# Kernel tuning notes

Hardware: AMD Instinct MI355X
Metric: run time of the kernel (lower is better)

Reference implementation:

```python
import jax, jax.numpy as jnp
import numpy as np

N_NODES = 50000
N_EDGES = 800000
D_NODE = 128
D_EDGE = 64
N_GC = 2
H = 256
N_GRAPHS = 512


def setup_inputs() -> dict:
    key = jax.random.key(0)
    ks = jax.random.split(key, 32)
    s = 0.05
    inp = {
        'x': jax.random.normal(ks[0], (N_NODES, D_NODE), jnp.float32),
        'edge_index': jax.random.randint(ks[1], (2, N_EDGES), 0, N_NODES, jnp.int64 if jax.config.jax_enable_x64 else jnp.int32),
        'edge_attr': jax.random.normal(ks[2], (N_EDGES, D_EDGE), jnp.float32),
        'batch': jnp.sort(jax.random.randint(ks[3], (N_NODES,), 0, N_GRAPHS)),
    }
    zin = 2 * D_NODE + D_EDGE  # 320
    inp['conv_Wf'] = jax.random.normal(ks[4], (N_GC, D_NODE, zin), jnp.float32) * s
    inp['conv_bf'] = jnp.zeros((N_GC, D_NODE), jnp.float32)
    inp['conv_Ws'] = jax.random.normal(ks[5], (N_GC, D_NODE, zin), jnp.float32) * s
    inp['conv_bs'] = jnp.zeros((N_GC, D_NODE), jnp.float32)
    # mlp_1: Linear(128->256), ReLU, Linear(256->256), ReLU, proj Linear(256->128)
    inp['mlp1_W0'] = jax.random.normal(ks[6], (H, D_NODE), jnp.float32) * s
    inp['mlp1_b0'] = jnp.zeros((H,), jnp.float32)
    inp['mlp1_W1'] = jax.random.normal(ks[7], (H, H), jnp.float32) * s
    inp['mlp1_b1'] = jnp.zeros((H,), jnp.float32)
    inp['mlp1_Wp'] = jax.random.normal(ks[8], (D_NODE, H), jnp.float32) * s
    inp['mlp1_bp'] = jnp.zeros((D_NODE,), jnp.float32)
    # mlp_2: same structure
    inp['mlp2_W0'] = jax.random.normal(ks[9], (H, D_NODE), jnp.float32) * s
    inp['mlp2_b0'] = jnp.zeros((H,), jnp.float32)
    inp['mlp2_W1'] = jax.random.normal(ks[10], (H, H), jnp.float32) * s
    inp['mlp2_b1'] = jnp.zeros((H,), jnp.float32)
    inp['mlp2_Wp'] = jax.random.normal(ks[11], (D_NODE, H), jnp.float32) * s
    inp['mlp2_bp'] = jnp.zeros((D_NODE,), jnp.float32)
    inp['out_W'] = jax.random.normal(ks[12], (1, D_NODE), jnp.float32) * s
    inp['out_b'] = jnp.zeros((1,), jnp.float32)
    return inp


def _mlp(x, W0, b0, W1, b1, Wp, bp):
    h = jax.nn.relu(x @ W0.T + b0)
    h = jax.nn.relu(h @ W1.T + b1)
    return h @ Wp.T + bp


def _cgconv(x, src, dst, edge_attr, Wf, bf, Ws, bs):
    # z = [x_i (target), x_j (source), edge_attr]  -> [E, 2D+De]
    z = jnp.concatenate([x[dst], x[src], edge_attr], axis=-1)
    msg = jax.nn.sigmoid(z @ Wf.T + bf) * jax.nn.softplus(z @ Ws.T + bs)
    aggr = jax.ops.segment_sum(msg, dst, num_segments=x.shape[0])
    return x + aggr  # CGConv residual


def reference(x, edge_index, edge_attr, batch,
              conv_Wf, conv_bf, conv_Ws, conv_bs,
              mlp1_W0, mlp1_b0, mlp1_W1, mlp1_b1, mlp1_Wp, mlp1_bp,
              mlp2_W0, mlp2_b0, mlp2_W1, mlp2_b1, mlp2_Wp, mlp2_bp,
              out_W, out_b):
    src, dst = edge_index[0], edge_index[1]
    out = x
    for l in range(N_GC):
        out = _cgconv(out, src, dst, edge_attr, conv_Wf[l], conv_bf[l], conv_Ws[l], conv_bs[l])
    out = out + _mlp(out, mlp1_W0, mlp1_b0, mlp1_W1, mlp1_b1, mlp1_Wp, mlp1_bp)
    out = jax.ops.segment_sum(out, batch, num_segments=N_GRAPHS)  # global_add_pool
    out = out + _mlp(out, mlp2_W0, mlp2_b0, mlp2_W1, mlp2_b1, mlp2_Wp, mlp2_bp)
    out = out @ out_W.T + out_b  # [n_graphs, 1]
    return out
```

## Files before the change

kernel.cpp:

```cpp
#include <hip/hip_runtime.h>
#include <stdint.h>

#define NN 50000
#define NE 800000
#define DN 128
#define DE 64
#define NG 512
#define HD 256
#define LDA 72
#define SPK_S 130

typedef unsigned short ushort_t;
typedef __attribute__((ext_vector_type(8))) short short8;
typedef __attribute__((ext_vector_type(4))) float floatx4;

__device__ __forceinline__ float bflo(unsigned u){ unsigned v=u<<16; float f; __builtin_memcpy(&f,&v,4); return f; }
__device__ __forceinline__ float bfhi(unsigned u){ unsigned v=u&0xffff0000u; float f; __builtin_memcpy(&f,&v,4); return f; }
__device__ __forceinline__ ushort_t f2bf(float f){ unsigned u; __builtin_memcpy(&u,&f,4); u += 0x7FFFu + ((u>>16)&1u); return (ushort_t)(u>>16); }
__device__ __forceinline__ unsigned cvtpk(float a, float b){
#if __has_builtin(__builtin_amdgcn_cvt_pk_bf16_f32)
  auto r = __builtin_amdgcn_cvt_pk_bf16_f32(a,b);
  unsigned u; __builtin_memcpy(&u,&r,4); return u;
#else
  return (unsigned)f2bf(a) | ((unsigned)f2bf(b)<<16);
#endif
}

__device__ __forceinline__ float actv(float fv, float sv){
  const float L2E = 1.44269504f, LN2 = 0.69314718f;
  float ef  = __builtin_amdgcn_exp2f(-L2E*fv);
  float sig = __builtin_amdgcn_rcpf(1.f+ef);
  float t   = __builtin_amdgcn_exp2f(-L2E*fabsf(sv));
  float sp  = fmaxf(sv,0.f) + LN2*__builtin_amdgcn_logf(1.f+t);
  return sig*sp;
}

__global__ void k_prep(const float* __restrict__ Wf, const float* __restrict__ Ws,
                       const float* __restrict__ W0, const float* __restrict__ W1, const float* __restrict__ Wp,
                       const float* __restrict__ cbf, const float* __restrict__ cbs,
                       ushort_t* Wnode, ushort_t* Wedge, ushort_t* W0b, ushort_t* W1b, ushort_t* Wpb,
                       float* bias512, int* deg){
  int i = blockIdx.x*256 + threadIdx.x;
  if(i < 131072){
    int l = i >> 16, r = i & 65535;
    int n = r >> 7, k = r & 127;
    const float* W = (n<256)? Wf : Ws;
    int nn = n & 127;
    int koff = ((n>>7)&1) ? 128+k : k;
    Wnode[i] = f2bf(W[(size_t)l*128*320 + (size_t)nn*320 + koff]);
  } else if(i < 163840){
    int j = i - 131072;
    int l = j >> 14, r = j & 16383;
    int n = r >> 6, k = r & 63;
    const float* W = (n<128)? Wf : Ws;
    int nn = n & 127;
    Wedge[j] = f2bf(W[(size_t)l*128*320 + (size_t)nn*320 + 256 + k]);
  } else if(i < 196608){
    int j = i - 163840; W0b[j] = f2bf(W0[j]);
  } else if(i < 262144){
    int j = i - 196608; W1b[j] = f2bf(W1[j]);
  } else if(i < 294912){
    int j = i - 262144; Wpb[j] = f2bf(Wp[j]);
  } else if(i < 295936){
    int j = i - 294912;
    int l = j >> 9, c = j & 511;
    float v = 0.f;
    if(c < 128) v = cbf[l*128 + c];
    else if(c >= 256 && c < 384) v = cbs[l*128 + (c-256)];
    bias512[j] = v;
  } else if(i < 295936 + NN){
    deg[i - 295936] = 0;
  }
}

__global__ void k_init_x(const float* x, float* xcur, ushort_t* xb){
  int i = blockIdx.x*256 + threadIdx.x;
  if(i < NN*DN){ float v = x[i]; xcur[i]=v; xb[i]=f2bf(v); }
}

__global__ void k_zero_u32(unsigned* p, int n){
  int i = blockIdx.x*256 + threadIdx.x;
  if(i<n) p[i]=0u;
}

__global__ void k_hist(const int* dst, int* deg){
  int i = blockIdx.x*256 + threadIdx.x;
  if(i<NE) atomicAdd(&deg[dst[i]], 1);
}

__global__ void k_blocksum(const int* deg, int* bsum, int n){
  __shared__ int s[256];
  int t = threadIdx.x, i = blockIdx.x*256 + t;
  s[t] = (i<n)? deg[i] : 0;
  __syncthreads();
  for(int o=128;o>0;o>>=1){ if(t<o) s[t]+=s[t+o]; __syncthreads(); }
  if(t==0) bsum[blockIdx.x]=s[0];
}

__global__ void k_scan_bsum(int* bsum, int nb, int* offs, int nnodes){
  __shared__ int s[2][256];
  int t = threadIdx.x;
  int v = (t<nb)? bsum[t] : 0;
  s[0][t]=v; __syncthreads();
  int cur=0;
  for(int o=1;o<256;o<<=1){
    int nx=cur^1;
    s[nx][t] = s[cur][t] + ((t>=o)? s[cur][t-o] : 0);
    cur=nx; __syncthreads();
  }
  if(t<nb) bsum[t] = s[cur][t] - v;
  if(t==255) offs[nnodes] = s[cur][255];
}

__global__ void k_scanscatter(const int* deg, const int* bsum, int* offs, int* cursor, int n){
  __shared__ int s[2][256];
  int t=threadIdx.x, i=blockIdx.x*256+t;
  int v=(i<n)? deg[i] : 0;
  s[0][t]=v; __syncthreads();
  int cur=0;
  for(int o=1;o<256;o<<=1){
    int nx=cur^1;
    s[nx][t] = s[cur][t] + ((t>=o)? s[cur][t-o] : 0);
    cur=nx; __syncthreads();
  }
  if(i<n){ int ex = s[cur][t]-v + bsum[blockIdx.x]; offs[i]=ex; cursor[i]=ex; }
}

__global__ void k_scatter(const int* dst, int* cursor, int* csr_pos){
  int i = blockIdx.x*256 + threadIdx.x;
  if(i<NE){ int pos = atomicAdd(&cursor[dst[i]], 1); csr_pos[i]=pos; }
}

__global__ __launch_bounds__(256) void k_permute(const float* __restrict__ ea,
      const int* __restrict__ src_g, const int* __restrict__ dst_g,
      const int* __restrict__ csr_pos,
      ushort_t* __restrict__ eab, int* __restrict__ src_csr, int* __restrict__ dst_csr){
  int id = blockIdx.x*256 + threadIdx.x;
  if(id >= NE*8) return;
  int e = id>>3, seg = id&7;
  int pos = csr_pos[e];
  const float4* p = (const float4*)&ea[(size_t)e*64 + seg*8];
  float4 f0 = p[0], f1 = p[1];
  uint4 q;
  q.x = cvtpk(f0.x,f0.y); q.y = cvtpk(f0.z,f0.w);
  q.z = cvtpk(f1.x,f1.y); q.w = cvtpk(f1.z,f1.w);
  *(uint4*)&eab[(size_t)pos*64 + seg*8] = q;
  if(seg==0){ src_csr[pos] = src_g[e]; dst_csr[pos] = dst_g[e]; }
}

__global__ __launch_bounds__(256) void k_gemm(const ushort_t* __restrict__ Ain, const ushort_t* __restrict__ Wg,
      int M, int N, int K, const float* __restrict__ bias, int mode,
      ushort_t* __restrict__ outb, float* __restrict__ outf, const float* __restrict__ addf){
  __shared__ __align__(16) ushort_t As[64*LDA];
  __shared__ __align__(16) ushort_t Bs[64*LDA];
  int tid = threadIdx.x;
  int m0 = blockIdx.x*64, n0 = blockIdx.y*64;
  int w = tid>>6, lane = tid&63, row16 = lane&15, quad = lane>>4;
  floatx4 acc[4];
  #pragma unroll
  for(int t=0;t<4;t++) acc[t]=(floatx4)(0.f);
  int nk = K>>6;
  for(int kc=0; kc<nk; kc++){
    #pragma unroll
    for(int i=0;i<2;i++){
      int lin = tid + i*256;
      int row = lin>>3, c8 = (lin&7)*8;
      uint4 va;
      int gm = m0+row;
      if(gm < M) va = *(const uint4*)&Ain[(size_t)gm*K + kc*64 + c8];
      else va = make_uint4(0,0,0,0);
      *(uint4*)&As[row*LDA + c8] = va;
      uint4 vb = *(const uint4*)&Wg[(size_t)(n0+row)*K + kc*64 + c8];
      *(uint4*)&Bs[row*LDA + c8] = vb;
    }
    __syncthreads();
    #pragma unroll
    for(int ks=0;ks<2;ks++){
      short8 a = *(const short8*)&As[(w*16+row16)*LDA + ks*32 + quad*8];
      #pragma unroll
      for(int t=0;t<4;t++){
        short8 b = *(const short8*)&Bs[(t*16+row16)*LDA + ks*32 + quad*8];
        acc[t] = __builtin_amdgcn_mfma_f32_16x16x32_bf16(a,b,acc[t],0,0,0);
      }
    }
    __syncthreads();
  }
  #pragma unroll
  for(int t=0;t<4;t++){
    int nn = n0 + t*16 + row16;
    #pragma unroll
    for(int r=0;r<4;r++){
      int m = m0 + w*16 + quad*4 + r;
      if(m>=M) continue;
      float v = acc[t][r];
      if(bias) v += bias[nn];
      if(mode==1){ v = v>0.f? v:0.f; outb[(size_t)m*N+nn]=f2bf(v); }
      else if(mode==2){ v += addf[(size_t)m*N+nn]; outf[(size_t)m*N+nn]=v; }
      else { outb[(size_t)m*N+nn]=f2bf(v); }
    }
  }
}

__global__ __launch_bounds__(256) void k_edge_msg(const ushort_t* __restrict__ eab_g,
      const int* __restrict__ src_csr, const int* __restrict__ dst_csr,
      const ushort_t* __restrict__ Wedge, const ushort_t* __restrict__ Atab,
      ushort_t* __restrict__ msg){
  __shared__ __align__(16) char smem[40960];
  ushort_t* We  = (ushort_t*)smem;
  unsigned* spk = (unsigned*)smem;
  ushort_t* el  = (ushort_t*)(smem + 32768);

  int tid = threadIdx.x;
  int e0 = blockIdx.x*64;
  {
    const uint4* s = (const uint4*)Wedge;
    #pragma unroll
    for(int i=0;i<8;i++){
      int g = tid + i*256;
      int row = g>>3, ch = g&7;
      int pch = ch ^ (row&7);
      *(uint4*)&We[row*64 + pch*8] = s[g];
    }
  }
  {
    const uint4* s = (const uint4*)eab_g + (size_t)e0*8;
    #pragma unroll
    for(int i=0;i<2;i++){
      int g = tid + i*256;
      int row = g>>3, ch = g&7;
      int pch = ch ^ (row&7);
      *(uint4*)&el[row*64 + pch*8] = s[g];
    }
  }
  __syncthreads();

  int w = tid>>6, lane = tid&63, row16 = lane&15, quad = lane>>4;
  floatx4 acc[16];
  #pragma unroll
  for(int t=0;t<16;t++) acc[t]=(floatx4)(0.f);
  #pragma unroll
  for(int ks=0;ks<2;ks++){
    int pch = (ks*4+quad) ^ (row16&7);
    short8 a = *(const short8*)&el[(w*16+row16)*64 + pch*8];
    #pragma unroll
    for(int t=0;t<16;t++){
      short8 b = *(const short8*)&We[(t*16+row16)*64 + pch*8];
      acc[t]=__builtin_amdgcn_mfma_f32_16x16x32_bf16(a,b,acc[t],0,0,0);
    }
  }
  __syncthreads();

  #pragma unroll
  for(int t=0;t<8;t++){
    int c = t*16 + row16;
    #pragma unroll
    for(int r=0;r<4;r++){
      int rl = w*16 + quad*4 + r;
      spk[rl*SPK_S + c] = cvtpk(acc[t][r], acc[t+8][r]);
    }
  }
  __syncthreads();

  #pragma unroll
  for(int j=0;j<4;j++){
    int id  = j*256 + tid;
    int eli = id >> 4;
    int c0  = (id & 15) * 8;
    int e   = e0 + eli;
    int d = dst_csr[e], s = src_csr[e];
    const unsigned* base = &spk[eli*SPK_S + c0];
    uint4 q0 = *(const uint4*)(base);
    uint4 q1 = *(const uint4*)(base + 4);
    const ushort_t* Adp = Atab + (size_t)d*512;
    const ushort_t* Asp = Atab + (size_t)s*512;
    uint4 a0 = *(const uint4*)&Adp[c0];
    uint4 a1 = *(const uint4*)&Asp[128+c0];
    uint4 a2 = *(const uint4*)&Adp[256+c0];
    uint4 a3 = *(const uint4*)&Asp[384+c0];
    unsigned qs[8] = {q0.x,q0.y,q0.z,q0.w,q1.x,q1.y,q1.z,q1.w};
    unsigned A0[4] = {a0.x,a0.y,a0.z,a0.w};
    unsigned A1[4] = {a1.x,a1.y,a1.z,a1.w};
    unsigned A2[4] = {a2.x,a2.y,a2.z,a2.w};
    unsigned A3[4] = {a3.x,a3.y,a3.z,a3.w};
    unsigned outw[4];
    #pragma unroll
    for(int k=0;k<4;k++){
      float fv0 = bflo(qs[2*k])   + bflo(A0[k]) + bflo(A1[k]);
      float sv0 = bfhi(qs[2*k])   + bflo(A2[k]) + bflo(A3[k]);
      float fv1 = bflo(qs[2*k+1]) + bfhi(A0[k]) + bfhi(A1[k]);
      float sv1 = bfhi(qs[2*k+1]) + bfhi(A2[k]) + bfhi(A3[k]);
      outw[k] = cvtpk(actv(fv0,sv0), actv(fv1,sv1));
    }
    uint4 o4; o4.x=outw[0]; o4.y=outw[1]; o4.z=outw[2]; o4.w=outw[3];
    *(uint4*)&msg[(size_t)e*128 + c0] = o4;
  }
}

__global__ __launch_bounds__(256) void k_aggregate(const ushort_t* __restrict__ msg,
      const int* __restrict__ offs, float* __restrict__ xcur, ushort_t* __restrict__ xb){
  int v = blockIdx.x*4 + (threadIdx.x>>6);
  int lane = threadIdx.x & 63;
  int rslot = lane>>4;
  int c0 = (lane&15)*8;
  int b = offs[v], e = offs[v+1];
  float acc[8];
  #pragma unroll
  for(int k=0;k<8;k++) acc[k]=0.f;
  for(int r=b+rslot; r<e; r+=4){
    uint4 m = *(const uint4*)&msg[(size_t)r*128 + c0];
    acc[0]+=bflo(m.x); acc[1]+=bfhi(m.x);
    acc[2]+=bflo(m.y); acc[3]+=bfhi(m.y);
    acc[4]+=bflo(m.z); acc[5]+=bfhi(m.z);
    acc[6]+=bflo(m.w); acc[7]+=bfhi(m.w);
  }
  #pragma unroll
  for(int k=0;k<8;k++){
    acc[k] += __shfl_xor(acc[k],16);
    acc[k] += __shfl_xor(acc[k],32);
  }
  if(rslot==0){
    float4 x0 = *(float4*)&xcur[(size_t)v*128+c0];
    float4 x1 = *(float4*)&xcur[(size_t)v*128+c0+4];
    x0.x+=acc[0]; x0.y+=acc[1]; x0.z+=acc[2]; x0.w+=acc[3];
    x1.x+=acc[4]; x1.y+=acc[5]; x1.z+=acc[6]; x1.w+=acc[7];
    *(float4*)&xcur[(size_t)v*128+c0]=x0;
    *(float4*)&xcur[(size_t)v*128+c0+4]=x1;
    uint4 o; o.x=cvtpk(x0.x,x0.y); o.y=cvtpk(x0.z,x0.w); o.z=cvtpk(x1.x,x1.y); o.w=cvtpk(x1.z,x1.w);
    *(uint4*)&xb[(size_t)v*128+c0]=o;
  }
}

__global__ __launch_bounds__(256) void k_pool(const float* __restrict__ xcur,
      const int* __restrict__ batch, float* __restrict__ pooled){
  int b0 = blockIdx.x * 128;
  int ch = threadIdx.x & 127;
  int half = threadIdx.x >> 7;
  int n0 = b0 + half*64;
  if(n0 >= NN) return;
  int n1 = n0 + 64; if(n1 > NN) n1 = NN;
  float sum = 0.f;
  int bid = batch[n0];
  for(int n=n0; n<n1; n++){
    int b = batch[n];
    if(b != bid){ atomicAdd(&pooled[(size_t)bid*128+ch], sum); sum=0.f; bid=b; }
    sum += xcur[(size_t)n*128 + ch];
  }
  atomicAdd(&pooled[(size_t)bid*128+ch], sum);
}

__global__ __launch_bounds__(256) void k_final(const float* __restrict__ pooled,
   const float* __restrict__ W0, const float* __restrict__ b0,
   const float* __restrict__ W1, const float* __restrict__ b1,
   const float* __restrict__ Wp, const float* __restrict__ bp,
   const float* __restrict__ outW, const float* __restrict__ outB,
   float* __restrict__ out){
  __shared__ float p[128], h0[256], h1[256], red[256];
  int g = blockIdx.x, t = threadIdx.x;
  if(t<128) p[t]=pooled[(size_t)g*128+t];
  __syncthreads();
  {
    const float4* wr = (const float4*)&W0[(size_t)t*128];
    float s=0.f;
    #pragma unroll 8
    for(int k=0;k<32;k++){ float4 wv=wr[k]; s += wv.x*p[k*4]+wv.y*p[k*4+1]+wv.z*p[k*4+2]+wv.w*p[k*4+3]; }
    s += b0[t]; h0[t] = s>0.f? s:0.f;
  }
  __syncthreads();
  {
    const float4* wr = (const float4*)&W1[(size_t)t*256];
    float s=0.f;
    #pragma unroll 8
    for(int k=0;k<64;k++){ float4 wv=wr[k]; s += wv.x*h0[k*4]+wv.y*h0[k*4+1]+wv.z*h0[k*4+2]+wv.w*h0[k*4+3]; }
    s += b1[t]; h1[t] = s>0.f? s:0.f;
  }
  __syncthreads();
  float rt = 0.f;
  if(t<128){
    const float4* wr=(const float4*)&Wp[(size_t)t*256];
    float s=0.f;
    #pragma unroll 8
    for(int k=0;k<64;k++){ float4 wv=wr[k]; s += wv.x*h1[k*4]+wv.y*h1[k*4+1]+wv.z*h1[k*4+2]+wv.w*h1[k*4+3]; }
    s += bp[t] + p[t];
    rt = s * outW[t];
  }
  red[t]=rt; __syncthreads();
  for(int o=128;o>0;o>>=1){ if(t<o) red[t]+=red[t+o]; __syncthreads(); }
  if(t==0) out[g] = red[0] + outB[0];
}

extern "C" void kernel_launch(void* const* d_in, const int* in_sizes, int n_in,
                              void* d_out, int out_size, void* d_ws, size_t ws_size,
                              hipStream_t stream){
  const float* x    = (const float*)d_in[0];
  const int*   ei   = (const int*)d_in[1];
  const float* ea   = (const float*)d_in[2];
  const int*   batch= (const int*)d_in[3];
  const float* cWf  = (const float*)d_in[4];
  const float* cbf  = (const float*)d_in[5];
  const float* cWs  = (const float*)d_in[6];
  const float* cbs  = (const float*)d_in[7];
  const float* W0   = (const float*)d_in[8];
  const float* b0   = (const float*)d_in[9];
  const float* W1   = (const float*)d_in[10];
  const float* b1   = (const float*)d_in[11];
  const float* Wp   = (const float*)d_in[12];
  const float* bp   = (const float*)d_in[13];
  const float* m2W0 = (const float*)d_in[14];
  const float* m2b0 = (const float*)d_in[15];
  const float* m2W1 = (const float*)d_in[16];
  const float* m2b1 = (const float*)d_in[17];
  const float* m2Wp = (const float*)d_in[18];
  const float* m2bp = (const float*)d_in[19];
  const float* outW = (const float*)d_in[20];
  const float* outB = (const float*)d_in[21];

  const int* srcp = ei;
  const int* dstp = ei + NE;

  char* ws = (char*)d_ws;
  size_t off = 0;
  auto alloc = [&](size_t bytes)->char*{
    char* p = ws + off;
    off += (bytes + 255) & ~(size_t)255;
    return p;
  };
  float*    xcur   = (float*)   alloc((size_t)NN*DN*4);
  ushort_t* xb     = (ushort_t*)alloc((size_t)NN*DN*2);
  ushort_t* Atab   = (ushort_t*)alloc((size_t)NN*512*2);
  ushort_t* msg    = (ushort_t*)alloc((size_t)NE*128*2);
  ushort_t* eab    = (ushort_t*)alloc((size_t)NE*64*2);
  ushort_t* Wnode  = (ushort_t*)alloc((size_t)2*512*128*2);
  ushort_t* Wedge  = (ushort_t*)alloc((size_t)2*256*64*2);
  ushort_t* W0b    = (ushort_t*)alloc((size_t)256*128*2);
  ushort_t* W1b    = (ushort_t*)alloc((size_t)256*256*2);
  ushort_t* Wpb    = (ushort_t*)alloc((size_t)128*256*2);
  float*    bias512= (float*)   alloc((size_t)2*512*4);
  int*      deg    = (int*)     alloc((size_t)NN*4);
  int*      offs   = (int*)     alloc((size_t)(NN+1)*4);
  int*      cursor = (int*)     alloc((size_t)NN*4);
  int*      csr_pos= (int*)     alloc((size_t)NE*4);
  int*      src_csr= (int*)     alloc((size_t)NE*4);
  int*      dst_csr= (int*)     alloc((size_t)NE*4);
  int*      bsum   = (int*)     alloc(256*4);
  float*    pooled = (float*)   alloc((size_t)NG*DN*4);
  ushort_t* h0 = Atab;
  ushort_t* h1 = Atab + (size_t)NN*256;

  k_prep<<<(295936+NN+255)/256, 256, 0, stream>>>(cWf, cWs, W0, W1, Wp, cbf, cbs,
                                   Wnode, Wedge, W0b, W1b, Wpb, bias512, deg);
  k_init_x<<<(NN*DN+255)/256, 256, 0, stream>>>(x, xcur, xb);

  int nb = (NN+255)/256;
  k_hist<<<(NE+255)/256, 256, 0, stream>>>(dstp, deg);
  k_blocksum<<<nb, 256, 0, stream>>>(deg, bsum, NN);
  k_scan_bsum<<<1, 256, 0, stream>>>(bsum, nb, offs, NN);
  k_scanscatter<<<nb, 256, 0, stream>>>(deg, bsum, offs, cursor, NN);
  k_scatter<<<(NE+255)/256, 256, 0, stream>>>(dstp, cursor, csr_pos);
  k_permute<<<(NE*8+255)/256, 256, 0, stream>>>(ea, srcp, dstp, csr_pos, eab, src_csr, dst_csr);

  for(int l=0;l<2;l++){
    dim3 ga((NN+63)/64, 512/64);
    k_gemm<<<ga, 256, 0, stream>>>(xb, Wnode + (size_t)l*512*128, NN, 512, 128,
                                   bias512 + l*512, 0, Atab, nullptr, nullptr);
    k_edge_msg<<<NE/64, 256, 0, stream>>>(eab, src_csr, dst_csr,
                                          Wedge + (size_t)l*256*64, Atab, msg);
    k_aggregate<<<NN/4, 256, 0, stream>>>(msg, offs, xcur, xb);
  }

  {
    dim3 g0((NN+63)/64, 256/64);
    k_gemm<<<g0, 256, 0, stream>>>(xb, W0b, NN, 256, 128, b0, 1, h0, nullptr, nullptr);
    dim3 g1((NN+63)/64, 256/64);
    k_gemm<<<g1, 256, 0, stream>>>(h0, W1b, NN, 256, 256, b1, 1, h1, nullptr, nullptr);
    dim3 g2((NN+63)/64, 128/64);
    k_gemm<<<g2, 256, 0, stream>>>(h1, Wpb, NN, 128, 256, bp, 2, nullptr, xcur, xcur);
  }

  k_zero_u32<<<(NG*DN+255)/256, 256, 0, stream>>>((unsigned*)pooled, NG*DN);
  k_pool<<<(NN+127)/128, 256, 0, stream>>>(xcur, batch, pooled);

  k_final<<<NG, 256, 0, stream>>>(pooled, m2W0, m2b0, m2W1, m2b1, m2Wp, m2bp,
                                  outW, outB, (float*)d_out);
  (void)in_sizes; (void)n_in; (void)out_size; (void)ws_size;
}
```

Before: 1.090 ms.

## Fuse edge aggregation into message kernel with segmented atomics, drop msg buffer

The edge message kernel now reduces the messages of consecutive dst-sorted edges in registers and adds them straight into xcur with float atomics. This removes the separate aggregate kernel and the large bf16 msg buffer that was written and then read back each layer. The edge-attribute permutation is folded into the first layer's message kernel through an edge-id gather, and the node GEMM now reads fp32 xcur and converts to bf16 on load, so the xb copy is gone. The shared-memory stride also changes. In exchange, summation order becomes nondeterministic and atomic traffic rises when a destination's edges span several groups.

```diff
diff --git a/kernel.cpp b/kernel.cpp
--- a/kernel.cpp
+++ b/kernel.cpp
@@ -8,7 +8,7 @@
 #define NG 512
 #define HD 256
 #define LDA 72
-#define SPK_S 130
+#define SPK_S 132
 
 typedef unsigned short ushort_t;
 typedef __attribute__((ext_vector_type(8))) short short8;
@@ -33,6 +33,10 @@
   float t   = __builtin_amdgcn_exp2f(-L2E*fabsf(sv));
   float sp  = fmaxf(sv,0.f) + LN2*__builtin_amdgcn_logf(1.f+t);
   return sig*sp;
+}
+
+__device__ __forceinline__ void atomAddF(float* p, float v){
+  unsafeAtomicAdd(p, v);
 }
 
 __global__ void k_prep(const float* __restrict__ Wf, const float* __restrict__ Ws,
@@ -73,9 +77,9 @@
   }
 }
 
-__global__ void k_init_x(const float* x, float* xcur, ushort_t* xb){
+__global__ void k_init_x(const float* x, float* xcur){
   int i = blockIdx.x*256 + threadIdx.x;
-  if(i < NN*DN){ float v = x[i]; xcur[i]=v; xb[i]=f2bf(v); }
+  if(i < NN*DN) xcur[i] = x[i];
 }
 
 __global__ void k_zero_u32(unsigned* p, int n){
@@ -126,29 +130,20 @@
   if(i<n){ int ex = s[cur][t]-v + bsum[blockIdx.x]; offs[i]=ex; cursor[i]=ex; }
 }
 
-__global__ void k_scatter(const int* dst, int* cursor, int* csr_pos){
+__global__ void k_scatter(const int* dst, const int* src, int* cursor,
+                          int* eid, int* src_csr, int* dst_csr){
   int i = blockIdx.x*256 + threadIdx.x;
-  if(i<NE){ int pos = atomicAdd(&cursor[dst[i]], 1); csr_pos[i]=pos; }
-}
-
-__global__ __launch_bounds__(256) void k_permute(const float* __restrict__ ea,
-      const int* __restrict__ src_g, const int* __restrict__ dst_g,
-      const int* __restrict__ csr_pos,
-      ushort_t* __restrict__ eab, int* __restrict__ src_csr, int* __restrict__ dst_csr){
-  int id = blockIdx.x*256 + threadIdx.x;
-  if(id >= NE*8) return;
-  int e = id>>3, seg = id&7;
-  int pos = csr_pos[e];
-  const float4* p = (const float4*)&ea[(size_t)e*64 + seg*8];
-  float4 f0 = p[0], f1 = p[1];
-  uint4 q;
-  q.x = cvtpk(f0.x,f0.y); q.y = cvtpk(f0.z,f0.w);
-  q.z = cvtpk(f1.x,f1.y); q.w = cvtpk(f1.z,f1.w);
-  *(uint4*)&eab[(size_t)pos*64 + seg*8] = q;
-  if(seg==0){ src_csr[pos] = src_g[e]; dst_csr[pos] = dst_g[e]; }
-}
-
-__global__ __launch_bounds__(256) void k_gemm(const ushort_t* __restrict__ Ain, const ushort_t* __restrict__ Wg,
+  if(i<NE){
+    int d = dst[i];
+    int pos = atomicAdd(&cursor[d], 1);
+    eid[pos] = i;
+    src_csr[pos] = src[i];
+    dst_csr[pos] = d;
+  }
+}
+
+__global__ __launch_bounds__(256) void k_gemm(const ushort_t* __restrict__ Ain,
+      const float* __restrict__ Af, const ushort_t* __restrict__ Wg,
       int M, int N, int K, const float* __restrict__ bias, int mode,
       ushort_t* __restrict__ outb, float* __restrict__ outf, const float* __restrict__ addf){
   __shared__ __align__(16) ushort_t As[64*LDA];
@@ -165,10 +160,18 @@
     for(int i=0;i<2;i++){
       int lin = tid + i*256;
       int row = lin>>3, c8 = (lin&7)*8;
-      uint4 va;
       int gm = m0+row;
-      if(gm < M) va = *(const uint4*)&Ain[(size_t)gm*K + kc*64 + c8];
-      else va = make_uint4(0,0,0,0);
+      uint4 va = make_uint4(0,0,0,0);
+      if(gm < M){
+        if(Af){
+          const float4* pf = (const float4*)&Af[(size_t)gm*K + kc*64 + c8];
+          float4 f0 = pf[0], f1 = pf[1];
+          va.x = cvtpk(f0.x,f0.y); va.y = cvtpk(f0.z,f0.w);
+          va.z = cvtpk(f1.x,f1.y); va.w = cvtpk(f1.z,f1.w);
+        } else {
+          va = *(const uint4*)&Ain[(size_t)gm*K + kc*64 + c8];
+        }
+      }
       *(uint4*)&As[row*LDA + c8] = va;
       uint4 vb = *(const uint4*)&Wg[(size_t)(n0+row)*K + kc*64 + c8];
       *(uint4*)&Bs[row*LDA + c8] = vb;
@@ -201,10 +204,11 @@
   }
 }
 
-__global__ __launch_bounds__(256) void k_edge_msg(const ushort_t* __restrict__ eab_g,
+__global__ __launch_bounds__(256) void k_edge_msg(const ushort_t* __restrict__ eab,
+      const float* __restrict__ ea, const int* __restrict__ eid,
       const int* __restrict__ src_csr, const int* __restrict__ dst_csr,
       const ushort_t* __restrict__ Wedge, const ushort_t* __restrict__ Atab,
-      ushort_t* __restrict__ msg){
+      float* __restrict__ xcur, ushort_t* __restrict__ eab_out, int first){
   __shared__ __align__(16) char smem[40960];
   ushort_t* We  = (ushort_t*)smem;
   unsigned* spk = (unsigned*)smem;
@@ -222,8 +226,23 @@
       *(uint4*)&We[row*64 + pch*8] = s[g];
     }
   }
-  {
-    const uint4* s = (const uint4*)eab_g + (size_t)e0*8;
+  if(first){
+    #pragma unroll
+    for(int i=0;i<2;i++){
+      int g = tid + i*256;
+      int row = g>>3, seg = g&7;
+      int eo = eid[e0+row];
+      const float4* p = (const float4*)&ea[(size_t)eo*64 + seg*8];
+      float4 f0 = p[0], f1 = p[1];
+      uint4 q;
+      q.x = cvtpk(f0.x,f0.y); q.y = cvtpk(f0.z,f0.w);
+      q.z = cvtpk(f1.x,f1.y); q.w = cvtpk(f1.z,f1.w);
+      int pch = seg ^ (row&7);
+      *(uint4*)&el[row*64 + pch*8] = q;
+      *(uint4*)&eab_out[(size_t)(e0+row)*64 + seg*8] = q;
+    }
+  } else {
+    const uint4* s = (const uint4*)eab + (size_t)e0*8;
     #pragma unroll
     for(int i=0;i<2;i++){
       int g = tid + i*256;
@@ -261,72 +280,54 @@
   }
   __syncthreads();
 
-  #pragma unroll
-  for(int j=0;j<4;j++){
-    int id  = j*256 + tid;
-    int eli = id >> 4;
-    int c0  = (id & 15) * 8;
-    int e   = e0 + eli;
-    int d = dst_csr[e], s = src_csr[e];
-    const unsigned* base = &spk[eli*SPK_S + c0];
-    uint4 q0 = *(const uint4*)(base);
-    uint4 q1 = *(const uint4*)(base + 4);
-    const ushort_t* Adp = Atab + (size_t)d*512;
-    const ushort_t* Asp = Atab + (size_t)s*512;
-    uint4 a0 = *(const uint4*)&Adp[c0];
-    uint4 a1 = *(const uint4*)&Asp[128+c0];
-    uint4 a2 = *(const uint4*)&Adp[256+c0];
-    uint4 a3 = *(const uint4*)&Asp[384+c0];
-    unsigned qs[8] = {q0.x,q0.y,q0.z,q0.w,q1.x,q1.y,q1.z,q1.w};
-    unsigned A0[4] = {a0.x,a0.y,a0.z,a0.w};
-    unsigned A1[4] = {a1.x,a1.y,a1.z,a1.w};
-    unsigned A2[4] = {a2.x,a2.y,a2.z,a2.w};
-    unsigned A3[4] = {a3.x,a3.y,a3.z,a3.w};
-    unsigned outw[4];
-    #pragma unroll
-    for(int k=0;k<4;k++){
-      float fv0 = bflo(qs[2*k])   + bflo(A0[k]) + bflo(A1[k]);
-      float sv0 = bfhi(qs[2*k])   + bflo(A2[k]) + bflo(A3[k]);
-      float fv1 = bflo(qs[2*k+1]) + bfhi(A0[k]) + bfhi(A1[k]);
-      float sv1 = bfhi(qs[2*k+1]) + bfhi(A2[k]) + bfhi(A3[k]);
-      outw[k] = cvtpk(actv(fv0,sv0), actv(fv1,sv1));
-    }
-    uint4 o4; o4.x=outw[0]; o4.y=outw[1]; o4.z=outw[2]; o4.w=outw[3];
-    *(uint4*)&msg[(size_t)e*128 + c0] = o4;
-  }
-}
-
-__global__ __launch_bounds__(256) void k_aggregate(const ushort_t* __restrict__ msg,
-      const int* __restrict__ offs, float* __restrict__ xcur, ushort_t* __restrict__ xb){
-  int v = blockIdx.x*4 + (threadIdx.x>>6);
-  int lane = threadIdx.x & 63;
-  int rslot = lane>>4;
-  int c0 = (lane&15)*8;
-  int b = offs[v], e = offs[v+1];
-  float acc[8];
-  #pragma unroll
-  for(int k=0;k<8;k++) acc[k]=0.f;
-  for(int r=b+rslot; r<e; r+=4){
-    uint4 m = *(const uint4*)&msg[(size_t)r*128 + c0];
-    acc[0]+=bflo(m.x); acc[1]+=bfhi(m.x);
-    acc[2]+=bflo(m.y); acc[3]+=bfhi(m.y);
-    acc[4]+=bflo(m.z); acc[5]+=bfhi(m.z);
-    acc[6]+=bflo(m.w); acc[7]+=bfhi(m.w);
-  }
-  #pragma unroll
-  for(int k=0;k<8;k++){
-    acc[k] += __shfl_xor(acc[k],16);
-    acc[k] += __shfl_xor(acc[k],32);
-  }
-  if(rslot==0){
-    float4 x0 = *(float4*)&xcur[(size_t)v*128+c0];
-    float4 x1 = *(float4*)&xcur[(size_t)v*128+c0+4];
-    x0.x+=acc[0]; x0.y+=acc[1]; x0.z+=acc[2]; x0.w+=acc[3];
-    x1.x+=acc[4]; x1.y+=acc[5]; x1.z+=acc[6]; x1.w+=acc[7];
-    *(float4*)&xcur[(size_t)v*128+c0]=x0;
-    *(float4*)&xcur[(size_t)v*128+c0+4]=x1;
-    uint4 o; o.x=cvtpk(x0.x,x0.y); o.y=cvtpk(x0.z,x0.w); o.z=cvtpk(x1.x,x1.y); o.w=cvtpk(x1.z,x1.w);
-    *(uint4*)&xb[(size_t)v*128+c0]=o;
+  {
+    int cc = tid & 15;
+    int grp = tid >> 4;
+    int c0 = cc*8;
+    int ebase = grp*4;
+    float a8[8];
+    #pragma unroll
+    for(int k=0;k<8;k++) a8[k]=0.f;
+    int dprev = dst_csr[e0 + ebase];
+    uint4 D0 = *(const uint4*)&Atab[(size_t)dprev*512 + c0];
+    uint4 D2 = *(const uint4*)&Atab[(size_t)dprev*512 + 256 + c0];
+    #pragma unroll
+    for(int j=0;j<4;j++){
+      int eli = ebase + j;
+      int e = e0 + eli;
+      int d = dst_csr[e], s = src_csr[e];
+      if(d != dprev){
+        float* xp = &xcur[(size_t)dprev*128 + c0];
+        #pragma unroll
+        for(int k=0;k<8;k++){ atomAddF(xp+k, a8[k]); a8[k]=0.f; }
+        dprev = d;
+        D0 = *(const uint4*)&Atab[(size_t)d*512 + c0];
+        D2 = *(const uint4*)&Atab[(size_t)d*512 + 256 + c0];
+      }
+      const ushort_t* Asp = Atab + (size_t)s*512;
+      uint4 S1 = *(const uint4*)&Asp[128+c0];
+      uint4 S3 = *(const uint4*)&Asp[384+c0];
+      const unsigned* base = &spk[eli*SPK_S + c0];
+      uint4 q0 = *(const uint4*)(base);
+      uint4 q1 = *(const uint4*)(base + 4);
+      unsigned qs[8] = {q0.x,q0.y,q0.z,q0.w,q1.x,q1.y,q1.z,q1.w};
+      unsigned Dx0[4] = {D0.x,D0.y,D0.z,D0.w};
+      unsigned Dx2[4] = {D2.x,D2.y,D2.z,D2.w};
+      unsigned Sx1[4] = {S1.x,S1.y,S1.z,S1.w};
+      unsigned Sx3[4] = {S3.x,S3.y,S3.z,S3.w};
+      #pragma unroll
+      for(int k=0;k<4;k++){
+        float fv0 = bflo(qs[2*k])   + bflo(Dx0[k]) + bflo(Sx1[k]);
+        float sv0 = bfhi(qs[2*k])   + bflo(Dx2[k]) + bflo(Sx3[k]);
+        float fv1 = bflo(qs[2*k+1]) + bfhi(Dx0[k]) + bfhi(Sx1[k]);
+        float sv1 = bfhi(qs[2*k+1]) + bfhi(Dx2[k]) + bfhi(Sx3[k]);
+        a8[2*k]   += actv(fv0,sv0);
+        a8[2*k+1] += actv(fv1,sv1);
+      }
+    }
+    float* xp = &xcur[(size_t)dprev*128 + c0];
+    #pragma unroll
+    for(int k=0;k<8;k++) atomAddF(xp+k, a8[k]);
   }
 }
 
@@ -425,9 +426,7 @@
     return p;
   };
   float*    xcur   = (float*)   alloc((size_t)NN*DN*4);
-  ushort_t* xb     = (ushort_t*)alloc((size_t)NN*DN*2);
   ushort_t* Atab   = (ushort_t*)alloc((size_t)NN*512*2);
-  ushort_t* msg    = (ushort_t*)alloc((size_t)NE*128*2);
   ushort_t* eab    = (ushort_t*)alloc((size_t)NE*64*2);
   ushort_t* Wnode  = (ushort_t*)alloc((size_t)2*512*128*2);
   ushort_t* Wedge  = (ushort_t*)alloc((size_t)2*256*64*2);
@@ -438,7 +437,7 @@
   int*      deg    = (int*)     alloc((size_t)NN*4);
   int*      offs   = (int*)     alloc((size_t)(NN+1)*4);
   int*      cursor = (int*)     alloc((size_t)NN*4);
-  int*      csr_pos= (int*)     alloc((size_t)NE*4);
+  int*      eid    = (int*)     alloc((size_t)NE*4);
   int*      src_csr= (int*)     alloc((size_t)NE*4);
   int*      dst_csr= (int*)     alloc((size_t)NE*4);
   int*      bsum   = (int*)     alloc(256*4);
@@ -448,32 +447,30 @@
 
   k_prep<<<(295936+NN+255)/256, 256, 0, stream>>>(cWf, cWs, W0, W1, Wp, cbf, cbs,
                                    Wnode, Wedge, W0b, W1b, Wpb, bias512, deg);
-  k_init_x<<<(NN*DN+255)/256, 256, 0, stream>>>(x, xcur, xb);
+  k_init_x<<<(NN*DN+255)/256, 256, 0, stream>>>(x, xcur);
 
   int nb = (NN+255)/256;
   k_hist<<<(NE+255)/256, 256, 0, stream>>>(dstp, deg);
   k_blocksum<<<nb, 256, 0, stream>>>(deg, bsum, NN);
   k_scan_bsum<<<1, 256, 0, stream>>>(bsum, nb, offs, NN);
   k_scanscatter<<<nb, 256, 0, stream>>>(deg, bsum, offs, cursor, NN);
-  k_scatter<<<(NE+255)/256, 256, 0, stream>>>(dstp, cursor, csr_pos);
-  k_permute<<<(NE*8+255)/256, 256, 0, stream>>>(ea, srcp, dstp, csr_pos, eab, src_csr, dst_csr);
+  k_scatter<<<(NE+255)/256, 256, 0, stream>>>(dstp, srcp, cursor, eid, src_csr, dst_csr);
 
   for(int l=0;l<2;l++){
     dim3 ga((NN+63)/64, 512/64);
-    k_gemm<<<ga, 256, 0, stream>>>(xb, Wnode + (size_t)l*512*128, NN, 512, 128,
+    k_gemm<<<ga, 256, 0, stream>>>(nullptr, xcur, Wnode + (size_t)l*512*128, NN, 512, 128,
                                    bias512 + l*512, 0, Atab, nullptr, nullptr);
-    k_edge_msg<<<NE/64, 256, 0, stream>>>(eab, src_csr, dst_csr,
-                                          Wedge + (size_t)l*256*64, Atab, msg);
-    k_aggregate<<<NN/4, 256, 0, stream>>>(msg, offs, xcur, xb);
+    k_edge_msg<<<NE/64, 256, 0, stream>>>(eab, ea, eid, src_csr, dst_csr,
+                                          Wedge + (size_t)l*256*64, Atab, xcur, eab, l==0?1:0);
   }
 
   {
     dim3 g0((NN+63)/64, 256/64);
-    k_gemm<<<g0, 256, 0, stream>>>(xb, W0b, NN, 256, 128, b0, 1, h0, nullptr, nullptr);
+    k_gemm<<<g0, 256, 0, stream>>>(nullptr, xcur, W0b, NN, 256, 128, b0, 1, h0, nullptr, nullptr);
     dim3 g1((NN+63)/64, 256/64);
-    k_gemm<<<g1, 256, 0, stream>>>(h0, W1b, NN, 256, 256, b1, 1, h1, nullptr, nullptr);
+    k_gemm<<<g1, 256, 0, stream>>>(h0, nullptr, W1b, NN, 256, 256, b1, 1, h1, nullptr, nullptr);
     dim3 g2((NN+63)/64, 128/64);
-    k_gemm<<<g2, 256, 0, stream>>>(h1, Wpb, NN, 128, 256, bp, 2, nullptr, xcur, xcur);
+    k_gemm<<<g2, 256, 0, stream>>>(h1, nullptr, Wpb, NN, 128, 256, bp, 2, nullptr, xcur, xcur);
   }
 
   k_zero_u32<<<(NG*DN+255)/256, 256, 0, stream>>>((unsigned*)pooled, NG*DN);
```

Result: slower. 2.763 ms (+153.4%).
